# Optimization experiments

Measured on AMD Instinct MI355X. Metric: run time of the kernel, lower is better.

## Reference

```python
import jax, jax.numpy as jnp
import numpy as np
import math

MAX_SEQ = 26
D = 7       # embedding dim
DA = 11     # attention / value dim
V = 29      # vocab size


def _pos_matrix():
    # Exact replica of get_pos_matrix(): denominator = 10000 ** (2*i/7), i in {0,2,4,6}
    store = np.zeros((MAX_SEQ, D), dtype=np.float32)
    for pos in range(MAX_SEQ):
        for i in range(0, D, 2):
            den = 10000 ** (2 * i / D)
            store[pos, i] = math.sin(pos / den)
            if i + 1 < D:
                store[pos, i + 1] = math.cos(pos / den)
    return jnp.asarray(store)


def setup_inputs() -> dict:
    key = jax.random.key(0)
    ks = jax.random.split(key, 20)

    def lin(k, out_f, in_f):
        kw, kb = jax.random.split(k)
        bound = 1.0 / np.sqrt(in_f)
        w = jax.random.uniform(kw, (out_f, in_f), jnp.float32, -bound, bound)
        b = jax.random.uniform(kb, (out_f,), jnp.float32, -bound, bound)
        return w, b

    x = jax.random.randint(ks[0], (MAX_SEQ,), 0, V)
    emb_table = jax.random.normal(ks[1], (V, D), jnp.float32)
    pos = _pos_matrix()

    w_k0, b_k0 = lin(ks[2], DA, D)
    w_q0, b_q0 = lin(ks[3], DA, D)
    w_v0, b_v0 = lin(ks[4], DA, D)
    w_f0, b_f0 = lin(ks[5], D, DA)
    w_k1, b_k1 = lin(ks[6], DA, D)
    w_q1, b_q1 = lin(ks[7], DA, D)
    w_v1, b_v1 = lin(ks[8], DA, D)
    w_f1, b_f1 = lin(ks[9], D, DA)
    w_out, b_out = lin(ks[10], V, D)

    return dict(x=x, emb_table=emb_table, pos=pos,
                w_k0=w_k0, b_k0=b_k0, w_q0=w_q0, b_q0=b_q0,
                w_v0=w_v0, b_v0=b_v0, w_f0=w_f0, b_f0=b_f0,
                w_k1=w_k1, b_k1=b_k1, w_q1=w_q1, b_q1=b_q1,
                w_v1=w_v1, b_v1=b_v1, w_f1=w_f1, b_f1=b_f1,
                w_out=w_out, b_out=b_out)


def _block(h, wk, bk, wq, bq, wv, bv, wf, bf):
    # h: [S, D] -> ([S, D], att [S, S])
    S = h.shape[0]
    k = h @ wk.T + bk  # [S, DA]
    q = h @ wq.T + bq
    v = h @ wv.T + bv
    att = q @ k.T      # [S, S], unscaled (as in the original)
    mask = jnp.tril(jnp.ones((S, S), dtype=bool))
    att = jnp.where(mask, att, -jnp.inf)
    att = jax.nn.softmax(att, axis=1)
    res = att @ v      # [S, DA]
    return res @ wf.T + bf, att


def reference(x, emb_table, pos,
              w_k0, b_k0, w_q0, b_q0, w_v0, b_v0, w_f0, b_f0,
              w_k1, b_k1, w_q1, b_q1, w_v1, b_v1, w_f1, b_f1,
              w_out, b_out):
    S = x.shape[0]
    emb = emb_table[x] + pos[:S]              # [S, D]
    h, _ = _block(emb, w_k0, b_k0, w_q0, b_q0, w_v0, b_v0, w_f0, b_f0)
    h, att = _block(h, w_k1, b_k1, w_q1, b_q1, w_v1, b_v1, w_f1, b_f1)
    out = h @ w_out.T + b_out                 # [S, V]
    return out, att
```

## Files before the change

kernel.cpp:

```cpp
#include <hip/hip_runtime.h>
#include <hip/hip_bf16.h>
#include <math.h>

#define S 26
#define D 7
#define DA 11
#define V 29
#define NT 256

__device__ __forceinline__ float dot8(float4 a0, float4 a1, float4 b0, float4 b1) {
    return a0.x*b0.x + a0.y*b0.y + a0.z*b0.z + a0.w*b0.w
         + a1.x*b1.x + a1.y*b1.y + a1.z*b1.z + a1.w*b1.w;
}
__device__ __forceinline__ float dot12(float4 a0, float4 a1, float4 a2,
                                       float4 b0, float4 b1, float4 b2) {
    return a0.x*b0.x + a0.y*b0.y + a0.z*b0.z + a0.w*b0.w
         + a1.x*b1.x + a1.y*b1.y + a1.z*b1.z + a1.w*b1.w
         + a2.x*b2.x + a2.y*b2.y + a2.z*b2.z + a2.w*b2.w;
}

__global__ __launch_bounds__(NT) void transformer_fwd(
    const int* __restrict__ x,
    const float* __restrict__ emb_table,
    const float* __restrict__ pos,
    const float* __restrict__ w_k0, const float* __restrict__ b_k0,
    const float* __restrict__ w_q0, const float* __restrict__ b_q0,
    const float* __restrict__ w_v0, const float* __restrict__ b_v0,
    const float* __restrict__ w_f0, const float* __restrict__ b_f0,
    const float* __restrict__ w_k1, const float* __restrict__ b_k1,
    const float* __restrict__ w_q1, const float* __restrict__ b_q1,
    const float* __restrict__ w_v1, const float* __restrict__ b_v1,
    const float* __restrict__ w_f1, const float* __restrict__ b_f1,
    const float* __restrict__ w_out, const float* __restrict__ b_out,
    float* __restrict__ out)
{
    __shared__ float4 wkv[2][12][2], wqv[2][12][2], wvv[2][12][2];
    __shared__ float4 wfv[2][8][3];
    __shared__ float4 wov[32][2];
    __shared__ float4 bkv[2][3], bqv[2][3], bvv[2][3], bfv[2][2];
    __shared__ float  bos[32];
    __shared__ float4 hv[S][2];
    __shared__ float4 kkv[28][3];
    __shared__ float4 qqv[S][3], vvv[S][3];
    __shared__ float4 attv[S][7];
    __shared__ float4 resv[S][3];

    const int t = threadIdx.x;

    {
        const int es = t >> 3, ed = t & 7;
        float hval = 0.f;
        if (t < S * 8) {
            if (ed < D) {
                const int xi = x[es];
                hval = emb_table[xi * D + ed] + pos[es * D + ed];
            }
            ((float*)hv)[t] = hval;
        }
        if (t < 96) {
            const int r = t >> 3, c = t & 7;
            const bool v = (r < DA) && (c < D);
            const int idx = r * D + c;
            ((float*)wkv[0])[t] = v ? w_k0[idx] : 0.f;
            ((float*)wkv[1])[t] = v ? w_k1[idx] : 0.f;
            ((float*)wqv[0])[t] = v ? w_q0[idx] : 0.f;
            ((float*)wqv[1])[t] = v ? w_q1[idx] : 0.f;
            ((float*)wvv[0])[t] = v ? w_v0[idx] : 0.f;
            ((float*)wvv[1])[t] = v ? w_v1[idx] : 0.f;
            const int rf = t / 12, cf = t % 12;
            const bool vf = (rf < D) && (cf < DA);
            const int idxf = rf * DA + cf;
            ((float*)wfv[0])[t] = vf ? w_f0[idxf] : 0.f;
            ((float*)wfv[1])[t] = vf ? w_f1[idxf] : 0.f;
        }
        {
            const int r = t >> 3, c = t & 7;
            const bool v = (r < V) && (c < D);
            ((float*)wov)[t] = v ? w_out[r * D + c] : 0.f;
        }
        if (t < 12) {
            ((float*)bkv[0])[t] = (t < DA) ? b_k0[t] : 0.f;
            ((float*)bkv[1])[t] = (t < DA) ? b_k1[t] : 0.f;
            ((float*)bqv[0])[t] = (t < DA) ? b_q0[t] : 0.f;
            ((float*)bqv[1])[t] = (t < DA) ? b_q1[t] : 0.f;
            ((float*)bvv[0])[t] = (t < DA) ? b_v0[t] : 0.f;
            ((float*)bvv[1])[t] = (t < DA) ? b_v1[t] : 0.f;
        }
        if (t < 8) {
            ((float*)bfv[0])[t] = (t < D) ? b_f0[t] : 0.f;
            ((float*)bfv[1])[t] = (t < D) ? b_f1[t] : 0.f;
        }
        if (t < 32) bos[t] = (t < V) ? b_out[t] : 0.f;
        if (t < 24) ((float*)kkv)[26 * 12 + t] = 0.f;
    }
    __syncthreads();

    for (int blk = 0; blk < 2; ++blk) {
        if (t < 234) {
            const int type = t / 78, rem = t % 78;
            const int r = rem / 3, c4 = rem % 3;
            const float4* W = (type == 0) ? &wkv[blk][0][0]
                             : (type == 1) ? &wqv[blk][0][0] : &wvv[blk][0][0];
            const float4  bb = ((type == 0) ? bkv[blk] : (type == 1) ? bqv[blk] : bvv[blk])[c4];
            const float4 h0 = hv[r][0], h1 = hv[r][1];
            const int c0 = c4 * 4;
            float4 o;
            o.x = dot8(h0, h1, W[(c0 + 0) * 2], W[(c0 + 0) * 2 + 1]) + bb.x;
            o.y = dot8(h0, h1, W[(c0 + 1) * 2], W[(c0 + 1) * 2 + 1]) + bb.y;
            o.z = dot8(h0, h1, W[(c0 + 2) * 2], W[(c0 + 2) * 2 + 1]) + bb.z;
            o.w = dot8(h0, h1, W[(c0 + 3) * 2], W[(c0 + 3) * 2 + 1]) + bb.w;
            float4* DST = (type == 0) ? &kkv[r][c4] : (type == 1) ? &qqv[r][c4] : &vvv[r][c4];
            *DST = o;
        }
        __syncthreads();

        if (t < 182) {
            const int r = t / 7, c4 = t % 7;
            const float4 q0 = qqv[r][0], q1 = qqv[r][1], q2 = qqv[r][2];
            float vo[4];
            #pragma unroll
            for (int cc = 0; cc < 4; ++cc) {
                const int c = c4 * 4 + cc;
                const float d = dot12(q0, q1, q2, kkv[c][0], kkv[c][1], kkv[c][2]);
                vo[cc] = (c <= r) ? d : 0.f;
            }
            attv[r][c4] = make_float4(vo[0], vo[1], vo[2], vo[3]);
        }
        __syncthreads();

        if (t < S) {
            float a[28];
            #pragma unroll
            for (int j = 0; j < 7; ++j) {
                const float4 aa = attv[t][j];
                a[4*j] = aa.x; a[4*j+1] = aa.y; a[4*j+2] = aa.z; a[4*j+3] = aa.w;
            }
            float m = a[0];
            #pragma unroll
            for (int c = 1; c < S; ++c) m = fmaxf(m, (c <= t) ? a[c] : -INFINITY);
            float e[S];
            float sum = 0.f;
            #pragma unroll
            for (int c = 0; c < S; ++c) {
                e[c] = (c <= t) ? __expf(a[c] - m) : 0.f;
                sum += e[c];
            }
            const float inv = 1.f / sum;
            #pragma unroll
            for (int j = 0; j < 7; ++j) {
                float4 o;
                o.x = e[4*j] * inv;
                o.y = (4*j+1 < S) ? e[4*j+1] * inv : 0.f;
                o.z = (4*j+2 < S) ? e[4*j+2] * inv : 0.f;
                o.w = (4*j+3 < S) ? e[4*j+3] * inv : 0.f;
                attv[t][j] = o;
            }
        }
        __syncthreads();

        if (blk == 1) {
            const float* atts = (const float*)attv;
            for (int i = t; i < S * S; i += NT) {
                const int r = i / S, c = i % S;
                out[S * V + i] = atts[r * 28 + c];
            }
        }

        if (t < 78) {
            const int r = t / 3, c4 = t % 3;
            float a[28];
            #pragma unroll
            for (int j = 0; j < 7; ++j) {
                const float4 aa = attv[r][j];
                a[4*j] = aa.x; a[4*j+1] = aa.y; a[4*j+2] = aa.z; a[4*j+3] = aa.w;
            }
            float4 acc = make_float4(0.f, 0.f, 0.f, 0.f);
            #pragma unroll
            for (int j = 0; j < S; ++j) {
                const float aj = a[j];
                const float4 vj = vvv[j][c4];
                acc.x += aj * vj.x; acc.y += aj * vj.y;
                acc.z += aj * vj.z; acc.w += aj * vj.w;
            }
            resv[r][c4] = acc;
        }
        __syncthreads();

        if (t < 52) {
            const int r = t >> 1, c4 = t & 1;
            const float4 r0 = resv[r][0], r1 = resv[r][1], r2 = resv[r][2];
            const float4 bb = bfv[blk][c4];
            const int c0 = c4 * 4;
            float4 o;
            o.x = dot12(r0, r1, r2, wfv[blk][c0+0][0], wfv[blk][c0+0][1], wfv[blk][c0+0][2]) + bb.x;
            o.y = dot12(r0, r1, r2, wfv[blk][c0+1][0], wfv[blk][c0+1][1], wfv[blk][c0+1][2]) + bb.y;
            o.z = dot12(r0, r1, r2, wfv[blk][c0+2][0], wfv[blk][c0+2][1], wfv[blk][c0+2][2]) + bb.z;
            o.w = dot12(r0, r1, r2, wfv[blk][c0+3][0], wfv[blk][c0+3][1], wfv[blk][c0+3][2]) + bb.w;
            hv[r][c4] = o;
        }
        __syncthreads();
    }

    if (t < 208) {
        const int r = t >> 3, c4 = t & 7;
        const float4 h0 = hv[r][0], h1 = hv[r][1];
        #pragma unroll
        for (int cc = 0; cc < 4; ++cc) {
            const int c = c4 * 4 + cc;
            const float d = dot8(h0, h1, wov[c][0], wov[c][1]) + bos[c];
            if (c < V) out[r * V + c] = d;
        }
    }
}

extern "C" void kernel_launch(void* const* d_in, const int* in_sizes, int n_in,
                              void* d_out, int out_size, void* d_ws, size_t ws_size,
                              hipStream_t stream) {
    const int*   x         = (const int*)  d_in[0];
    const float* emb_table = (const float*)d_in[1];
    const float* pos       = (const float*)d_in[2];
    const float* w_k0 = (const float*)d_in[3];  const float* b_k0 = (const float*)d_in[4];
    const float* w_q0 = (const float*)d_in[5];  const float* b_q0 = (const float*)d_in[6];
    const float* w_v0 = (const float*)d_in[7];  const float* b_v0 = (const float*)d_in[8];
    const float* w_f0 = (const float*)d_in[9];  const float* b_f0 = (const float*)d_in[10];
    const float* w_k1 = (const float*)d_in[11]; const float* b_k1 = (const float*)d_in[12];
    const float* w_q1 = (const float*)d_in[13]; const float* b_q1 = (const float*)d_in[14];
    const float* w_v1 = (const float*)d_in[15]; const float* b_v1 = (const float*)d_in[16];
    const float* w_f1 = (const float*)d_in[17]; const float* b_f1 = (const float*)d_in[18];
    const float* w_out = (const float*)d_in[19]; const float* b_out = (const float*)d_in[20];
    float* out = (float*)d_out;

    transformer_fwd<<<1, NT, 0, stream>>>(
        x, emb_table, pos,
        w_k0, b_k0, w_q0, b_q0, w_v0, b_v0, w_f0, b_f0,
        w_k1, b_k1, w_q1, b_q1, w_v1, b_v1, w_f1, b_f1,
        w_out, b_out, out);
}
```

Baseline: 12.22 us.

## Fuse attention scores, softmax, AV, projection and output into one register phase

Scores, causal softmax, attention-times-V, the output projection and the final vocab projection now run inside a single phase. Each row is handled by a pair of lanes that combine partial results with warp shuffles instead of going through shared-memory buffers. This removes the attv/resv scratch arrays and several __syncthreads barriers per block, which should cut serialization in this latency-bound single-block kernel. In exchange only 52 threads do work in that phase, each with more serial arithmetic, and the attention output writes are strided per thread.

```diff
diff --git a/kernel.cpp b/kernel.cpp
--- a/kernel.cpp
+++ b/kernel.cpp
@@ -40,10 +40,8 @@
     __shared__ float4 bkv[2][3], bqv[2][3], bvv[2][3], bfv[2][2];
     __shared__ float  bos[32];
     __shared__ float4 hv[S][2];
-    __shared__ float4 kkv[28][3];
+    __shared__ float4 kkv[S][3];
     __shared__ float4 qqv[S][3], vvv[S][3];
-    __shared__ float4 attv[S][7];
-    __shared__ float4 resv[S][3];
 
     const int t = threadIdx.x;
 
@@ -91,7 +89,6 @@
             ((float*)bfv[1])[t] = (t < D) ? b_f1[t] : 0.f;
         }
         if (t < 32) bos[t] = (t < V) ? b_out[t] : 0.f;
-        if (t < 24) ((float*)kkv)[26 * 12 + t] = 0.f;
     }
     __syncthreads();
 
@@ -114,102 +111,87 @@
         }
         __syncthreads();
 
-        if (t < 182) {
-            const int r = t / 7, c4 = t % 7;
-            const float4 q0 = qqv[r][0], q1 = qqv[r][1], q2 = qqv[r][2];
-            float vo[4];
-            #pragma unroll
-            for (int cc = 0; cc < 4; ++cc) {
-                const int c = c4 * 4 + cc;
-                const float d = dot12(q0, q1, q2, kkv[c][0], kkv[c][1], kkv[c][2]);
-                vo[cc] = (c <= r) ? d : 0.f;
+        {
+            const int w = t >> 6, lane = t & 63;
+            const int pr = lane >> 1, half = lane & 1;
+            const int r = w * 13 + pr;
+            if (w < 2 && pr < 13) {
+                const float4 q0 = qqv[r][0], q1 = qqv[r][1], q2 = qqv[r][2];
+                const int cbase = half << 4;
+                float p[16];
+                float m = -INFINITY;
+                #pragma unroll
+                for (int jj = 0; jj < 16; ++jj) {
+                    const int c = cbase + jj;
+                    const int ck = (c > 25) ? 25 : c;
+                    const float d = dot12(q0, q1, q2, kkv[ck][0], kkv[ck][1], kkv[ck][2]);
+                    p[jj] = (c <= r) ? d : -INFINITY;
+                    m = fmaxf(m, p[jj]);
+                }
+                m = fmaxf(m, __shfl_xor(m, 1));
+                float sum = 0.f;
+                #pragma unroll
+                for (int jj = 0; jj < 16; ++jj) {
+                    p[jj] = __expf(p[jj] - m);
+                    sum += p[jj];
+                }
+                sum += __shfl_xor(sum, 1);
+                const float inv = 1.f / sum;
+                #pragma unroll
+                for (int jj = 0; jj < 16; ++jj) p[jj] *= inv;
+
+                if (blk == 1) {
+                    #pragma unroll
+                    for (int jj = 0; jj < 16; ++jj) {
+                        const int c = cbase + jj;
+                        if (c < S) out[S * V + r * S + c] = p[jj];
+                    }
+                }
+
+                float4 a0 = make_float4(0.f,0.f,0.f,0.f), a1 = a0, a2 = a0;
+                #pragma unroll
+                for (int jj = 0; jj < 16; ++jj) {
+                    const int j = cbase + jj;
+                    const int jv = (j > 25) ? 25 : j;
+                    const float aj = p[jj];
+                    const float4 v0 = vvv[jv][0], v1 = vvv[jv][1], v2 = vvv[jv][2];
+                    a0.x += aj*v0.x; a0.y += aj*v0.y; a0.z += aj*v0.z; a0.w += aj*v0.w;
+                    a1.x += aj*v1.x; a1.y += aj*v1.y; a1.z += aj*v1.z; a1.w += aj*v1.w;
+                    a2.x += aj*v2.x; a2.y += aj*v2.y; a2.z += aj*v2.z; a2.w += aj*v2.w;
+                }
+                a0.x += __shfl_xor(a0.x, 1); a0.y += __shfl_xor(a0.y, 1);
+                a0.z += __shfl_xor(a0.z, 1); a0.w += __shfl_xor(a0.w, 1);
+                a1.x += __shfl_xor(a1.x, 1); a1.y += __shfl_xor(a1.y, 1);
+                a1.z += __shfl_xor(a1.z, 1); a1.w += __shfl_xor(a1.w, 1);
+                a2.x += __shfl_xor(a2.x, 1); a2.y += __shfl_xor(a2.y, 1);
+                a2.z += __shfl_xor(a2.z, 1); a2.w += __shfl_xor(a2.w, 1);
+
+                const int c0 = half * 4;
+                const float4 bb = bfv[blk][half];
+                float4 h4;
+                h4.x = dot12(a0,a1,a2, wfv[blk][c0+0][0], wfv[blk][c0+0][1], wfv[blk][c0+0][2]) + bb.x;
+                h4.y = dot12(a0,a1,a2, wfv[blk][c0+1][0], wfv[blk][c0+1][1], wfv[blk][c0+1][2]) + bb.y;
+                h4.z = dot12(a0,a1,a2, wfv[blk][c0+2][0], wfv[blk][c0+2][1], wfv[blk][c0+2][2]) + bb.z;
+                h4.w = dot12(a0,a1,a2, wfv[blk][c0+3][0], wfv[blk][c0+3][1], wfv[blk][c0+3][2]) + bb.w;
+
+                if (blk == 0) {
+                    hv[r][half] = h4;
+                } else {
+                    float4 oth;
+                    oth.x = __shfl_xor(h4.x, 1); oth.y = __shfl_xor(h4.y, 1);
+                    oth.z = __shfl_xor(h4.z, 1); oth.w = __shfl_xor(h4.w, 1);
+                    const float4 hh0 = half ? oth : h4;
+                    const float4 hh1 = half ? h4 : oth;
+                    #pragma unroll
+                    for (int jj = 0; jj < 16; ++jj) {
+                        const int c = cbase + jj;
+                        const float d = dot8(hh0, hh1, wov[c][0], wov[c][1]) + bos[c];
+                        if (c < V) out[r * V + c] = d;
+                    }
+                }
             }
-            attv[r][c4] = make_float4(vo[0], vo[1], vo[2], vo[3]);
-        }
-        __syncthreads();
-
-        if (t < S) {
-            float a[28];
-            #pragma unroll
-            for (int j = 0; j < 7; ++j) {
-                const float4 aa = attv[t][j];
-                a[4*j] = aa.x; a[4*j+1] = aa.y; a[4*j+2] = aa.z; a[4*j+3] = aa.w;
-            }
-            float m = a[0];
-            #pragma unroll
-            for (int c = 1; c < S; ++c) m = fmaxf(m, (c <= t) ? a[c] : -INFINITY);
-            float e[S];
-            float sum = 0.f;
-            #pragma unroll
-            for (int c = 0; c < S; ++c) {
-                e[c] = (c <= t) ? __expf(a[c] - m) : 0.f;
-                sum += e[c];
-            }
-            const float inv = 1.f / sum;
-            #pragma unroll
-            for (int j = 0; j < 7; ++j) {
-                float4 o;
-                o.x = e[4*j] * inv;
-                o.y = (4*j+1 < S) ? e[4*j+1] * inv : 0.f;
-                o.z = (4*j+2 < S) ? e[4*j+2] * inv : 0.f;
-                o.w = (4*j+3 < S) ? e[4*j+3] * inv : 0.f;
-                attv[t][j] = o;
-            }
-        }
-        __syncthreads();
-
-        if (blk == 1) {
-            const float* atts = (const float*)attv;
-            for (int i = t; i < S * S; i += NT) {
-                const int r = i / S, c = i % S;
-                out[S * V + i] = atts[r * 28 + c];
-            }
-        }
-
-        if (t < 78) {
-            const int r = t / 3, c4 = t % 3;
-            float a[28];
-            #pragma unroll
-            for (int j = 0; j < 7; ++j) {
-                const float4 aa = attv[r][j];
-                a[4*j] = aa.x; a[4*j+1] = aa.y; a[4*j+2] = aa.z; a[4*j+3] = aa.w;
-            }
-            float4 acc = make_float4(0.f, 0.f, 0.f, 0.f);
-            #pragma unroll
-            for (int j = 0; j < S; ++j) {
-                const float aj = a[j];
-                const float4 vj = vvv[j][c4];
-                acc.x += aj * vj.x; acc.y += aj * vj.y;
-                acc.z += aj * vj.z; acc.w += aj * vj.w;
-            }
-            resv[r][c4] = acc;
-        }
-        __syncthreads();
-
-        if (t < 52) {
-            const int r = t >> 1, c4 = t & 1;
-            const float4 r0 = resv[r][0], r1 = resv[r][1], r2 = resv[r][2];
-            const float4 bb = bfv[blk][c4];
-            const int c0 = c4 * 4;
-            float4 o;
-            o.x = dot12(r0, r1, r2, wfv[blk][c0+0][0], wfv[blk][c0+0][1], wfv[blk][c0+0][2]) + bb.x;
-            o.y = dot12(r0, r1, r2, wfv[blk][c0+1][0], wfv[blk][c0+1][1], wfv[blk][c0+1][2]) + bb.y;
-            o.z = dot12(r0, r1, r2, wfv[blk][c0+2][0], wfv[blk][c0+2][1], wfv[blk][c0+2][2]) + bb.z;
-            o.w = dot12(r0, r1, r2, wfv[blk][c0+3][0], wfv[blk][c0+3][1], wfv[blk][c0+3][2]) + bb.w;
-            hv[r][c4] = o;
-        }
-        __syncthreads();
-    }
-
-    if (t < 208) {
-        const int r = t >> 3, c4 = t & 7;
-        const float4 h0 = hv[r][0], h1 = hv[r][1];
-        #pragma unroll
-        for (int cc = 0; cc < 4; ++cc) {
-            const int c = c4 * 4 + cc;
-            const float d = dot8(h0, h1, wov[c][0], wov[c][1]) + bos[c];
-            if (c < V) out[r * V + c] = d;
-        }
+        }
+        if (blk == 0) __syncthreads();
     }
 }
 
```

New measurement: 14.17 us. 15.9% more time.
